# Kernel tuning notes

Hardware: AMD Instinct MI355X
Metric: run time of the kernel (lower is better)

## Reference

```python
import jax, jax.numpy as jnp
import numpy as np

N = 2097152
POS_DIM, H1, C_MID, C_IN, C_OUT = 3, 16, 64, 1, 64


def setup_inputs() -> dict:
    key = jax.random.key(0)
    ks = jax.random.split(key, 9)
    def lin(kw, kb, fan_in, fan_out):
        bound = 1.0 / np.sqrt(fan_in)
        w = jax.random.uniform(kw, (fan_in, fan_out), jnp.float32, -bound, bound)
        b = jax.random.uniform(kb, (fan_out,), jnp.float32, -bound, bound)
        return w, b
    w11, b11 = lin(ks[0], ks[1], POS_DIM, H1)
    w12, b12 = lin(ks[2], ks[3], H1, C_MID)
    w13, b13 = lin(ks[4], ks[5], C_MID, C_OUT * C_IN)
    return {
        "x": jax.random.normal(ks[6], (N, C_IN), jnp.float32),
        "pos_i": jax.random.normal(ks[7], (N, POS_DIM), jnp.float32),
        "pos_j": jax.random.normal(ks[8], (N, POS_DIM), jnp.float32),
        "w11": w11, "b11": b11,
        "w12": w12, "b12": b12,
        "w13": w13, "b13": b13,
    }


def reference(x, pos_i, pos_j, w11, b11, w12, b12, w13, b13) -> jnp.ndarray:
    # per-point MLP on relative position -> dynamic weight matrix W [N, c_in, c_out]
    pos_local = pos_j - pos_i                      # [N, 3]
    h = jax.nn.celu(pos_local @ w11 + b11)         # [N, 16]
    h = jax.nn.celu(h @ w12 + b12)                 # [N, 64]
    W = (h @ w13 + b13).reshape(-1, C_IN, C_OUT)   # [N, 1, 64]
    # bmm: x[:, None, :] @ W -> [N, 1, c_out] -> squeeze -> [N, c_out]
    out = jnp.einsum('ni,nio->no', x, W)
    return out
```

## Files before the change

kernel.cpp:

```cpp
#include <hip/hip_runtime.h>


typedef __attribute__((ext_vector_type(8))) _Float16 f16x8;
typedef __attribute__((ext_vector_type(4))) float f32x4;

#define TILES 4

__device__ __forceinline__ float celu1(float a) {
    return a > 0.0f ? a : __expf(a) - 1.0f;
}

__global__ __launch_bounds__(256) void centershift_kernel(
    const float* __restrict__ x,
    const float* __restrict__ pos_i,
    const float* __restrict__ pos_j,
    const float* __restrict__ w11, const float* __restrict__ b11,
    const float* __restrict__ w12, const float* __restrict__ b12,
    const float* __restrict__ w13, const float* __restrict__ b13,
    float* __restrict__ out, int n)
{
    __shared__ __align__(16) _Float16 h2s[4][64 * 64];
    __shared__ __align__(16) float    stg[4][1024];

    const int lane = threadIdx.x & 63;
    const int wid  = threadIdx.x >> 6;
    const int g    = lane >> 4;
    const int r16  = lane & 15;

    const int wbase = (blockIdx.x * 4 + wid) * (64 * TILES);
    if (wbase >= n) return;

    char* h2b  = (char*)&h2s[wid][0];
    char* stgb = (char*)&stg[wid][0];

    f16x8 a3[4][2];
#pragma unroll
    for (int u = 0; u < 4; ++u)
#pragma unroll
        for (int kh = 0; kh < 2; ++kh) {
            f16x8 v;
#pragma unroll
            for (int j = 0; j < 8; ++j)
                v[j] = (_Float16)w13[(kh * 32 + g * 8 + j) * 64 + u * 16 + r16];
            a3[u][kh] = v;
        }
    float b3v[4][4];
#pragma unroll
    for (int u = 0; u < 4; ++u) {
        const float4 bv = *reinterpret_cast<const float4*>(b13 + u * 16 + g * 4);
        b3v[u][0] = bv.x; b3v[u][1] = bv.y; b3v[u][2] = bv.z; b3v[u][3] = bv.w;
    }

    const float* pip = pos_i + 3 * (size_t)(wbase + lane);
    const float* pjp = pos_j + 3 * (size_t)(wbase + lane);
    float3 cpi = *reinterpret_cast<const float3*>(pip);
    float3 cpj = *reinterpret_cast<const float3*>(pjp);

    const int swzW = (lane & 7) << 4;
    const int rowW = lane * 128;
    const int swzR = (r16 & 7) << 4;

#pragma unroll 1
    for (int t = 0; t < TILES; ++t) {
        const int tb = wbase + t * 64;
        if (tb >= n) break;

        const float p0 = cpj.x - cpi.x, p1 = cpj.y - cpi.y, p2 = cpj.z - cpi.z;

        float h1[16];
#pragma unroll
        for (int j = 0; j < 16; ++j) {
            float a = b11[j];
            a = fmaf(p0, w11[j], a);
            a = fmaf(p1, w11[16 + j], a);
            a = fmaf(p2, w11[32 + j], a);
            h1[j] = celu1(a);
        }

        if (t + 1 < TILES) {
            cpi = *reinterpret_cast<const float3*>(pip + (t + 1) * 192);
            cpj = *reinterpret_cast<const float3*>(pjp + (t + 1) * 192);
        }

        for (int c = 0; c < 8; ++c) {
            f16x8 v;
#pragma unroll
            for (int j = 0; j < 8; ++j) {
                const int o = c * 8 + j;
                float a = b12[o];
#pragma unroll
                for (int k = 0; k < 16; ++k)
                    a = fmaf(h1[k], w12[k * 64 + o], a);
                v[j] = (_Float16)celu1(a);
            }
            *reinterpret_cast<f16x8*>(h2b + (rowW + ((c * 16) ^ swzW))) = v;
        }

#pragma unroll
        for (int t2 = 0; t2 < 4; ++t2) {
            const int pt   = t2 * 16 + r16;
            const int rowR = pt * 128;
            const f16x8 bb0 = *reinterpret_cast<const f16x8*>(h2b + (rowR + ((     g * 16) ^ swzR)));
            const f16x8 bb1 = *reinterpret_cast<const f16x8*>(h2b + (rowR + ((64 + g * 16) ^ swzR)));
            const float xvt = x[tb + pt];
#pragma unroll
            for (int u = 0; u < 4; ++u) {
                f32x4 acc = { b3v[u][0], b3v[u][1], b3v[u][2], b3v[u][3] };
                acc = __builtin_amdgcn_mfma_f32_16x16x32_f16(a3[u][0], bb0, acc, 0, 0, 0);
                acc = __builtin_amdgcn_mfma_f32_16x16x32_f16(a3[u][1], bb1, acc, 0, 0, 0);
                float4 o4 = { acc[0] * xvt, acc[1] * xvt, acc[2] * xvt, acc[3] * xvt };
                const int wb = r16 * 256 + (((u * 64 + g * 16)) ^ ((r16 & 7) << 4));
                *reinterpret_cast<float4*>(stgb + wb) = o4;
            }
            float* og = out + (size_t)(tb + t2 * 16) * 64;
#pragma unroll
            for (int k = 0; k < 4; ++k) {
                const int ptl = k * 4 + (lane >> 4);
                const int c   = lane & 15;
                const int rb  = ptl * 256 + ((c * 16) ^ ((ptl & 7) << 4));
                const float4 v = *reinterpret_cast<const float4*>(stgb + rb);
                *reinterpret_cast<float4*>(og + k * 256 + lane * 4) = v;
            }
        }
    }
}

extern "C" void kernel_launch(void* const* d_in, const int* in_sizes, int n_in,
                              void* d_out, int out_size, void* d_ws, size_t ws_size,
                              hipStream_t stream) {
    const float* x     = (const float*)d_in[0];
    const float* pos_i = (const float*)d_in[1];
    const float* pos_j = (const float*)d_in[2];
    const float* w11   = (const float*)d_in[3];
    const float* b11   = (const float*)d_in[4];
    const float* w12   = (const float*)d_in[5];
    const float* b12   = (const float*)d_in[6];
    const float* w13   = (const float*)d_in[7];
    const float* b13   = (const float*)d_in[8];
    float* out = (float*)d_out;

    const int n = in_sizes[0];
    const int per_block = 256 * TILES;
    const int blocks = (n + per_block - 1) / per_block;
    centershift_kernel<<<blocks, 256, 0, stream>>>(
        x, pos_i, pos_j, w11, b11, w12, b12, w13, b13, out, n);
}
```

Baseline: 146.2 us.

## Compute second MLP layer with MFMA instead of scalar FMAs

```diff
diff --git a/kernel.cpp b/kernel.cpp
--- a/kernel.cpp
+++ b/kernel.cpp
@@ -20,18 +20,19 @@
     float* __restrict__ out, int n)
 {
     __shared__ __align__(16) _Float16 h2s[4][64 * 64];
-    __shared__ __align__(16) float    stg[4][1024];
+    __shared__ __align__(16) char     aux[4][4096];
 
     const int lane = threadIdx.x & 63;
     const int wid  = threadIdx.x >> 6;
     const int g    = lane >> 4;
     const int r16  = lane & 15;
+    const int swzR = (r16 & 7) << 4;
 
     const int wbase = (blockIdx.x * 4 + wid) * (64 * TILES);
     if (wbase >= n) return;
 
     char* h2b  = (char*)&h2s[wid][0];
-    char* stgb = (char*)&stg[wid][0];
+    char* auxb = (char*)&aux[wid][0];
 
     f16x8 a3[4][2];
 #pragma unroll
@@ -44,21 +45,28 @@
                 v[j] = (_Float16)w13[(kh * 32 + g * 8 + j) * 64 + u * 16 + r16];
             a3[u][kh] = v;
         }
-    float b3v[4][4];
+    f16x8 a2[4];
 #pragma unroll
-    for (int u = 0; u < 4; ++u) {
-        const float4 bv = *reinterpret_cast<const float4*>(b13 + u * 16 + g * 4);
-        b3v[u][0] = bv.x; b3v[u][1] = bv.y; b3v[u][2] = bv.z; b3v[u][3] = bv.w;
+    for (int u2 = 0; u2 < 4; ++u2) {
+        f16x8 v;
+#pragma unroll
+        for (int j = 0; j < 8; ++j) {
+            const int k = g * 8 + j;
+            v[j] = (k < 16) ? (_Float16)w12[k * 64 + u2 * 16 + r16] : (_Float16)0.0f;
+        }
+        a2[u2] = v;
+    }
+    float b2v[4][4];
+#pragma unroll
+    for (int u2 = 0; u2 < 4; ++u2) {
+        const float4 bv = *reinterpret_cast<const float4*>(b12 + u2 * 16 + g * 4);
+        b2v[u2][0] = bv.x; b2v[u2][1] = bv.y; b2v[u2][2] = bv.z; b2v[u2][3] = bv.w;
     }
 
     const float* pip = pos_i + 3 * (size_t)(wbase + lane);
     const float* pjp = pos_j + 3 * (size_t)(wbase + lane);
     float3 cpi = *reinterpret_cast<const float3*>(pip);
     float3 cpj = *reinterpret_cast<const float3*>(pjp);
-
-    const int swzW = (lane & 7) << 4;
-    const int rowW = lane * 128;
-    const int swzR = (r16 & 7) << 4;
 
 #pragma unroll 1
     for (int t = 0; t < TILES; ++t) {
@@ -76,24 +84,35 @@
             a = fmaf(p2, w11[32 + j], a);
             h1[j] = celu1(a);
         }
+        {
+            f16x8 hp0, hp1;
+#pragma unroll
+            for (int j = 0; j < 8; ++j) { hp0[j] = (_Float16)h1[j]; hp1[j] = (_Float16)h1[8 + j]; }
+            *reinterpret_cast<f16x8*>(auxb + lane * 48)      = hp0;
+            *reinterpret_cast<f16x8*>(auxb + lane * 48 + 16) = hp1;
+        }
 
         if (t + 1 < TILES) {
             cpi = *reinterpret_cast<const float3*>(pip + (t + 1) * 192);
             cpj = *reinterpret_cast<const float3*>(pjp + (t + 1) * 192);
         }
 
-        for (int c = 0; c < 8; ++c) {
-            f16x8 v;
 #pragma unroll
-            for (int j = 0; j < 8; ++j) {
-                const int o = c * 8 + j;
-                float a = b12[o];
+        for (int tt = 0; tt < 4; ++tt) {
+            const int pt = tt * 16 + r16;
+            const f16x8 bfrag = *reinterpret_cast<const f16x8*>(auxb + pt * 48 + (g & 1) * 16);
 #pragma unroll
-                for (int k = 0; k < 16; ++k)
-                    a = fmaf(h1[k], w12[k * 64 + o], a);
-                v[j] = (_Float16)celu1(a);
+            for (int u2 = 0; u2 < 4; ++u2) {
+                f32x4 acc = { b2v[u2][0], b2v[u2][1], b2v[u2][2], b2v[u2][3] };
+                acc = __builtin_amdgcn_mfma_f32_16x16x32_f16(a2[u2], bfrag, acc, 0, 0, 0);
+                union { _Float16 h[4]; unsigned long long v; } pk;
+                pk.h[0] = (_Float16)celu1(acc[0]);
+                pk.h[1] = (_Float16)celu1(acc[1]);
+                pk.h[2] = (_Float16)celu1(acc[2]);
+                pk.h[3] = (_Float16)celu1(acc[3]);
+                const int byteoff = pt * 128 + u2 * 32 + g * 8;
+                *reinterpret_cast<unsigned long long*>(h2b + (byteoff ^ swzR)) = pk.v;
             }
-            *reinterpret_cast<f16x8*>(h2b + (rowW + ((c * 16) ^ swzW))) = v;
         }
 
 #pragma unroll
@@ -105,12 +124,13 @@
             const float xvt = x[tb + pt];
 #pragma unroll
             for (int u = 0; u < 4; ++u) {
-                f32x4 acc = { b3v[u][0], b3v[u][1], b3v[u][2], b3v[u][3] };
+                const float4 bias = *reinterpret_cast<const float4*>(b13 + u * 16 + g * 4);
+                f32x4 acc = { bias.x, bias.y, bias.z, bias.w };
                 acc = __builtin_amdgcn_mfma_f32_16x16x32_f16(a3[u][0], bb0, acc, 0, 0, 0);
                 acc = __builtin_amdgcn_mfma_f32_16x16x32_f16(a3[u][1], bb1, acc, 0, 0, 0);
                 float4 o4 = { acc[0] * xvt, acc[1] * xvt, acc[2] * xvt, acc[3] * xvt };
-                const int wb = r16 * 256 + (((u * 64 + g * 16)) ^ ((r16 & 7) << 4));
-                *reinterpret_cast<float4*>(stgb + wb) = o4;
+                const int wb = r16 * 256 + ((u * 64 + g * 16) ^ ((r16 & 7) << 4));
+                *reinterpret_cast<float4*>(auxb + wb) = o4;
             }
             float* og = out + (size_t)(tb + t2 * 16) * 64;
 #pragma unroll
@@ -118,7 +138,7 @@
                 const int ptl = k * 4 + (lane >> 4);
                 const int c   = lane & 15;
                 const int rb  = ptl * 256 + ((c * 16) ^ ((ptl & 7) << 4));
-                const float4 v = *reinterpret_cast<const float4*>(stgb + rb);
+                const float4 v = *reinterpret_cast<const float4*>(auxb + rb);
                 *reinterpret_cast<float4*>(og + k * 256 + lane * 4) = v;
             }
         }
```

After: 175.5 us. 1.2x slower.
